# Performance work log

Hardware: AMD Instinct MI355X
Metric: run time of the kernel (lower is better)

The kernel has to match this reference:

```python
import jax, jax.numpy as jnp
import numpy as np

D_MODEL = 1024
N_HEADS = 16
HEAD_DIM = D_MODEL // N_HEADS


def setup_inputs() -> dict:
    key = jax.random.key(0)
    k1, k2, k3, k4, k5 = jax.random.split(key, 5)
    B, S = 2, 2048
    x = jax.random.normal(k1, (B, S, D_MODEL), dtype=jnp.float32)
    mask = jnp.ones((B, 1, S), dtype=jnp.int32)
    s1 = 1.0 / np.sqrt(D_MODEL)
    qkv_w = jax.random.normal(k2, (3 * D_MODEL, D_MODEL), dtype=jnp.float32) * s1
    qkv_b = jax.random.normal(k3, (3 * D_MODEL,), dtype=jnp.float32) * 0.02
    wo_w = jax.random.normal(k4, (D_MODEL, D_MODEL), dtype=jnp.float32) * s1
    wo_b = jax.random.normal(k5, (D_MODEL,), dtype=jnp.float32) * 0.02
    return {"x": x, "mask": mask, "qkv_w": qkv_w, "qkv_b": qkv_b, "wo_w": wo_w, "wo_b": wo_b}


def reference(x, mask, qkv_w, qkv_b, wo_w, wo_b):
    B, S, _ = x.shape
    # fused QKV projection: [B,S,3d]
    qkv = jnp.einsum('bsd,ed->bse', x, qkv_w) + qkv_b
    qkv = qkv.reshape(B, S, 3, N_HEADS, HEAD_DIM).transpose(2, 0, 3, 1, 4)
    q, k, v = qkv[0], qkv[1], qkv[2]  # each [B,H,S,hd]
    scores = jnp.einsum('bhsd,bhtd->bhst', q, k) / np.sqrt(HEAD_DIM)
    # mask [B,1,S] -> [B,1,1,S]; fill -inf where mask == 0
    scores = jnp.where(mask[:, None] == 0, -jnp.inf, scores)
    weights = jax.nn.softmax(scores, axis=-1)  # dropout p=0.0 -> identity
    out = jnp.einsum('bhst,bhtd->bhsd', weights, v)
    out = out.transpose(0, 2, 1, 3).reshape(B, S, D_MODEL)
    out = jnp.einsum('bsd,ed->bse', out, wo_w) + wo_b
    return out, weights
```

## Files before the change

### kernel.cpp

```cpp
#include <hip/hip_runtime.h>
#include <cstdint>
#include <cstddef>

typedef unsigned short u16;
typedef __attribute__((ext_vector_type(8))) short bf16x8;
typedef __attribute__((ext_vector_type(4))) float f32x4;

#define DEV static __device__ __forceinline__

DEV void gload_lds16(const void* g, void* l) {
  __builtin_amdgcn_global_load_lds((const __attribute__((address_space(1))) void*)g,
                                   (__attribute__((address_space(3))) void*)l, 16, 0, 0);
}

DEV u16 f2bf(float f) {
  unsigned x = __float_as_uint(f);
  return (u16)((x + 0x7FFFu + ((x >> 16) & 1u)) >> 16);
}

DEV unsigned cvtpk(float lo, float hi) {
  unsigned r;
  asm("v_cvt_pk_bf16_f32 %0, %1, %2" : "=v"(r) : "v"(lo), "v"(hi));
  return r;
}

#if __has_builtin(__builtin_amdgcn_exp2f)
DEV float fexp2(float x) { return __builtin_amdgcn_exp2f(x); }
#else
DEV float fexp2(float x) { return exp2f(x); }
#endif

#define WAITV(n)                                                   \
  do {                                                             \
    asm volatile("s_waitcnt vmcnt(" #n ")" ::: "memory");          \
    __builtin_amdgcn_sched_barrier(0);                             \
  } while (0)

DEV void sbar() {
  __builtin_amdgcn_sched_barrier(0);
  __builtin_amdgcn_s_barrier();
  __builtin_amdgcn_sched_barrier(0);
}

__global__ __launch_bounds__(256) void cvt3(const float* __restrict__ a, u16* __restrict__ da,
                                            const float* __restrict__ b, u16* __restrict__ db,
                                            const float* __restrict__ c, u16* __restrict__ dc,
                                            const int* __restrict__ mask,
                                            unsigned* __restrict__ mpack) {
  int bid = blockIdx.x;
  if (bid == 8192) {
    const int j = threadIdx.x;
    if (j < 128) {
      const int* mb = mask + (j >> 6) * 2048 + (j & 63) * 32;
      unsigned bits = 0;
      for (int k = 0; k < 32; ++k) bits |= (mb[k] != 0 ? 1u : 0u) << k;
      mpack[j] = bits;
    }
    return;
  }
  const float* s;
  u16* d;
  int base;
  if (bid < 4096) { s = a; d = da; base = bid; }
  else if (bid < 7168) { s = b; d = db; base = bid - 4096; }
  else { s = c; d = dc; base = bid - 7168; }
  const int i = (base * 256 + (int)threadIdx.x) * 4;
  float4 v = *(const float4*)(s + i);
  uint2 p;
  p.x = (unsigned)f2bf(v.x) | ((unsigned)f2bf(v.y) << 16);
  p.y = (unsigned)f2bf(v.z) | ((unsigned)f2bf(v.w) << 16);
  *(uint2*)(d + i) = p;
}

template <int EPI, int BM, int BN>
__global__ __launch_bounds__(256) void gemm_bt(const u16* __restrict__ A,
                                               const u16* __restrict__ Bm,
                                               const float* __restrict__ bias,
                                               void* __restrict__ Cout,
                                               u16* __restrict__ Vt,
                                               int M, int N, int K) {
  __shared__ u16 As[2][BM * 32];
  __shared__ u16 Bs[2][BN * 32];
  constexpr int MT = BM / 32, NT = BN / 32;
  const int cpx = (int)gridDim.x >> 3;
  const int bid = ((int)blockIdx.x & 7) * cpx + ((int)blockIdx.x >> 3);
  const int nb = N / BN;
  const int m0 = (bid / nb) * BM;
  const int n0 = (bid % nb) * BN;
  const int tid = threadIdx.x;
  const int w = tid >> 6, lane = tid & 63;
  const int wm = (w >> 1) * (BM / 2), wn = (w & 1) * (BN / 2);
  const int lr = lane & 15, lg = lane >> 4;

  f32x4 acc[MT][NT];
  const f32x4 z4 = {0.f, 0.f, 0.f, 0.f};
#pragma unroll
  for (int m = 0; m < MT; ++m)
#pragma unroll
    for (int n = 0; n < NT; ++n) acc[m][n] = z4;

  auto stage = [&](int ks, int buf) {
    const int k0 = ks << 5;
#pragma unroll
    for (int i = 0; i < BM * 4 / 256; ++i) {
      const int o = i * 256 + tid;
      const int row = o >> 2, c = o & 3;
      gload_lds16(A + (size_t)(m0 + row) * K + k0 + c * 8, &As[buf][(i * 256 + w * 64) * 8]);
    }
#pragma unroll
    for (int i = 0; i < BN * 4 / 256; ++i) {
      const int o = i * 256 + tid;
      const int row = o >> 2, c = o & 3;
      gload_lds16(Bm + (size_t)(n0 + row) * K + k0 + c * 8, &Bs[buf][(i * 256 + w * 64) * 8]);
    }
  };

  const int nk = K >> 5;
  stage(0, 0);
  __syncthreads();
  for (int ks = 0; ks < nk; ++ks) {
    const int cur = ks & 1;
    if (ks + 1 < nk) stage(ks + 1, cur ^ 1);
    bf16x8 af[MT], bfr[NT];
#pragma unroll
    for (int m = 0; m < MT; ++m)
      af[m] = *(const bf16x8*)&As[cur][(wm + m * 16 + lr) * 32 + lg * 8];
#pragma unroll
    for (int n = 0; n < NT; ++n)
      bfr[n] = *(const bf16x8*)&Bs[cur][(wn + n * 16 + lr) * 32 + lg * 8];
    __builtin_amdgcn_s_setprio(1);
#pragma unroll
    for (int m = 0; m < MT; ++m)
#pragma unroll
      for (int n = 0; n < NT; ++n)
        acc[m][n] = __builtin_amdgcn_mfma_f32_16x16x32_bf16(af[m], bfr[n], acc[m][n], 0, 0, 0);
    __builtin_amdgcn_s_setprio(0);
    __syncthreads();
  }

#pragma unroll
  for (int n = 0; n < NT; ++n) {
    const int e = n0 + wn + n * 16 + lr;
    const float bv = bias[e];
    if (EPI == 1 && (e >> 10) == 2) {
      const int h = (e >> 6) & 15, d = e & 63;
#pragma unroll
      for (int m = 0; m < MT; ++m) {
        const int row0 = m0 + wm + m * 16 + lg * 4;
        const int bb = row0 >> 11, s0 = row0 & 2047;
        uint2 pv;
        pv.x = cvtpk(acc[m][n][0] + bv, acc[m][n][1] + bv);
        pv.y = cvtpk(acc[m][n][2] + bv, acc[m][n][3] + bv);
        *(uint2*)(Vt + (size_t)(bb * 16 + h) * 131072 + (size_t)d * 2048 + s0) = pv;
      }
    } else {
#pragma unroll
      for (int m = 0; m < MT; ++m) {
#pragma unroll
        for (int r = 0; r < 4; ++r) {
          const int row = m0 + wm + m * 16 + lg * 4 + r;
          const float v = acc[m][n][r] + bv;
          if (EPI == 0) {
            ((float*)Cout)[(size_t)row * N + e] = v;
          } else {
            const int which = e >> 10, h = (e >> 6) & 15, d = e & 63;
            const int bb = row >> 11, s = row & 2047;
            ((u16*)Cout)[(size_t)which * 4194304 +
                         (((size_t)(bb * 16 + h) * 2048 + s) << 6) + d] = f2bf(v);
          }
        }
      }
    }
  }
}

__global__ __launch_bounds__(256, 4) void attn(const u16* __restrict__ Q,
                                               const u16* __restrict__ Kg,
                                               const u16* __restrict__ Vtg,
                                               const unsigned* __restrict__ mpack,
                                               float* __restrict__ Wout,
                                               u16* __restrict__ Og) {
  __shared__ u16 Ks[2][4096];
  __shared__ u16 Vs[2][4096];
  __shared__ float Pf[4][512];
  const int L = ((int)blockIdx.x & 7) * 128 + ((int)blockIdx.x >> 3);
  const int bh = L >> 5, qt = L & 31;
  const int b = bh >> 4, h = bh & 15;
  const int tid = threadIdx.x;
  const int w = tid >> 6, lane = tid & 63;
  const int lr = lane & 15, lg = lane >> 4;
  const int srow0 = qt * 64 + w * 16;
  const float C2 = 0.18033688011112042f;
  const float M2 = 11.541560327111707f;

  const u16* qrow = Q + ((size_t)bh * 2048 + srow0 + lr) * 64;
  const bf16x8 qf0 = *(const bf16x8*)(qrow + lg * 8);
  const bf16x8 qf1 = *(const bf16x8*)(qrow + 32 + lg * 8);
  const unsigned* mpk = mpack + b * 64;

  auto stageK = [&](int kt, u16* dst) {
    const u16* g = Kg + (size_t)bh * 131072 + (size_t)kt * 4096;
#pragma unroll
    for (int iss = 0; iss < 2; ++iss) {
      const int o = iss * 256 + tid;
      const int row = o >> 3, c = o & 7;
      gload_lds16(g + row * 64 + ((c ^ (row & 7)) << 3), dst + (iss * 256 + w * 64) * 8);
    }
  };
  auto stageV = [&](int kt, u16* dst) {
    const u16* g = Vtg + (size_t)bh * 131072 + kt * 64;
#pragma unroll
    for (int iss = 0; iss < 2; ++iss) {
      const int o = iss * 256 + tid;
      const int row = o >> 3, c = o & 7;
      gload_lds16(g + (size_t)row * 2048 + ((c ^ (row & 7)) << 3),
                  dst + (iss * 256 + w * 64) * 8);
    }
  };
  auto qk = [&](const u16* kb, f32x4* sc) {
    const f32x4 z4 = {0.f, 0.f, 0.f, 0.f};
    __builtin_amdgcn_s_setprio(1);
#pragma unroll
    for (int n = 0; n < 4; ++n) {
      const int tr = n * 16 + lr;
      const bf16x8 k0 = *(const bf16x8*)&kb[tr * 64 + ((lg ^ (tr & 7)) << 3)];
      const bf16x8 k1 = *(const bf16x8*)&kb[tr * 64 + (((lg + 4) ^ (tr & 7)) << 3)];
      f32x4 s = z4;
      s = __builtin_amdgcn_mfma_f32_16x16x32_bf16(k0, qf0, s, 0, 0, 0);
      s = __builtin_amdgcn_mfma_f32_16x16x32_bf16(k1, qf1, s, 0, 0, 0);
      sc[n] = s;
    }
    __builtin_amdgcn_s_setprio(0);
  };

  stageK(0, &Ks[0][0]);
  stageK(1, &Ks[1][0]);
  WAITV(2);
  sbar();
  float lsum = 0.f;
  int cur3 = 0, stg3 = 2;
  for (int t = 0; t < 32; ++t) {
    u16* curb = (cur3 == 0) ? &Ks[0][0] : ((cur3 == 1) ? &Ks[1][0] : &Vs[0][0]);
    const unsigned mx = mpk[t * 2], my = mpk[t * 2 + 1];
    if (t + 2 < 32) {
      u16* stb = (stg3 == 0) ? &Ks[0][0] : ((stg3 == 1) ? &Ks[1][0] : &Vs[0][0]);
      stageK(t + 2, stb);
    }
    f32x4 sc[4];
    qk(curb, sc);
    f32x4 p[4];
#pragma unroll
    for (int n = 0; n < 4; ++n)
#pragma unroll
      for (int r = 0; r < 4; ++r) p[n][r] = fexp2(fmaf(sc[n][r], C2, -M2));
    if ((mx & my) != 0xFFFFFFFFu) {
#pragma unroll
      for (int n = 0; n < 4; ++n) {
        const unsigned wsel = (n < 2) ? mx : my;
#pragma unroll
        for (int r = 0; r < 4; ++r) {
          const unsigned bit = (wsel >> ((n & 1) * 16 + lg * 4 + r)) & 1u;
          p[n][r] = bit ? p[n][r] : 0.f;
        }
      }
    }
#pragma unroll
    for (int n = 0; n < 4; ++n) lsum += (p[n][0] + p[n][1]) + (p[n][2] + p[n][3]);
    if (t + 1 < 32) {
      if (t + 2 < 32) {
        WAITV(2);
      } else {
        WAITV(0);
      }
      sbar();
    }
    cur3 = (cur3 == 2) ? 0 : cur3 + 1;
    stg3 = (stg3 == 2) ? 0 : stg3 + 1;
  }
  lsum += __shfl_xor(lsum, 16);
  lsum += __shfl_xor(lsum, 32);
  const float rl = 1.0f / lsum;

  sbar();
  f32x4 oacc[4];
  const f32x4 z4 = {0.f, 0.f, 0.f, 0.f};
#pragma unroll
  for (int n = 0; n < 4; ++n) oacc[n] = z4;

  float* Wb = Wout + (size_t)bh * 2048 * 2048;
  char* pfw = (char*)&Pf[w][0];
  const int sw = (lr & 7) << 4;
  const int ql0 = lane >> 3, ch = lane & 7;

  stageK(0, &Ks[0][0]);
  stageV(0, &Vs[0][0]);
  WAITV(0);
  sbar();
  for (int t = 0; t < 32; ++t) {
    const int cur = t & 1;
    const unsigned mx = mpk[t * 2], my = mpk[t * 2 + 1];
    if (t + 1 < 32) {
      stageK(t + 1, &Ks[cur ^ 1][0]);
      stageV(t + 1, &Vs[cur ^ 1][0]);
    }
    f32x4 sc[4];
    qk(&Ks[cur][0], sc);
    f32x4 wv[4];
#pragma unroll
    for (int n = 0; n < 4; ++n)
#pragma unroll
      for (int r = 0; r < 4; ++r) wv[n][r] = fexp2(fmaf(sc[n][r], C2, -M2)) * rl;
    if ((mx & my) != 0xFFFFFFFFu) {
#pragma unroll
      for (int n = 0; n < 4; ++n) {
        const unsigned wsel = (n < 2) ? mx : my;
#pragma unroll
        for (int r = 0; r < 4; ++r) {
          const unsigned bit = (wsel >> ((n & 1) * 16 + lg * 4 + r)) & 1u;
          wv[n][r] = bit ? wv[n][r] : 0.f;
        }
      }
    }
#pragma unroll
    for (int hh = 0; hh < 2; ++hh) {
      *(f32x4*)(pfw + (lr * 128 + ((lg * 16) ^ sw))) = wv[2 * hh];
      *(f32x4*)(pfw + (lr * 128 + ((64 + lg * 16) ^ sw))) = wv[2 * hh + 1];
#pragma unroll
      for (int s2 = 0; s2 < 2; ++s2) {
        const int ql = s2 * 8 + ql0;
        const f32x4 rv = *(const f32x4*)(pfw + (ql * 128 + ((ch * 16) ^ ((ql & 7) << 4))));
        __builtin_nontemporal_store(
            rv, (f32x4*)(Wb + (size_t)(srow0 + ql) * 2048 + t * 64 + hh * 32 + ch * 4));
      }
      const f32x4 a0 = *(const f32x4*)(pfw + (lr * 128 + ((lg * 32) ^ sw)));
      const f32x4 a1 = *(const f32x4*)(pfw + (lr * 128 + ((lg * 32 + 16) ^ sw)));
      int4 pk4;
      pk4.x = cvtpk(a0[0], a0[1]);
      pk4.y = cvtpk(a0[2], a0[3]);
      pk4.z = cvtpk(a1[0], a1[1]);
      pk4.w = cvtpk(a1[2], a1[3]);
      const bf16x8 pfr = *(const bf16x8*)&pk4;
      __builtin_amdgcn_s_setprio(1);
#pragma unroll
      for (int n = 0; n < 4; ++n) {
        const int dr = n * 16 + lr;
        const bf16x8 vf = *(const bf16x8*)&Vs[cur][dr * 64 + (((lg + hh * 4) ^ (dr & 7)) << 3)];
        oacc[n] = __builtin_amdgcn_mfma_f32_16x16x32_bf16(pfr, vf, oacc[n], 0, 0, 0);
      }
      __builtin_amdgcn_s_setprio(0);
    }
    if (t + 1 < 32) {
      WAITV(4);
      sbar();
    }
  }

#pragma unroll
  for (int n = 0; n < 4; ++n)
#pragma unroll
    for (int r = 0; r < 4; ++r) {
      const int s = srow0 + lg * 4 + r;
      Og[((size_t)(b * 2048 + s)) * 1024 + h * 64 + n * 16 + lr] = f2bf(oacc[n][r]);
    }
}

extern "C" void kernel_launch(void* const* d_in, const int* in_sizes, int n_in,
                              void* d_out, int out_size, void* d_ws, size_t ws_size,
                              hipStream_t stream) {
  const float* x     = (const float*)d_in[0];
  const int*   mask  = (const int*)d_in[1];
  const float* qkv_w = (const float*)d_in[2];
  const float* qkv_b = (const float*)d_in[3];
  const float* wo_w  = (const float*)d_in[4];
  const float* wo_b  = (const float*)d_in[5];
  float* out = (float*)d_out;

  char* ws = (char*)d_ws;
  u16* xb   = (u16*)(ws);
  u16* qwb  = (u16*)(ws + (8u << 20));
  u16* wob  = (u16*)(ws + (14u << 20));
  u16* qkvb = (u16*)(ws + (16u << 20));
  unsigned* mpack = (unsigned*)(ws + (16u << 20) + 16777216);
  u16* vt   = (u16*)(ws + (40u << 20));
  u16* ob   = (u16*)(ws + (48u << 20));

  cvt3<<<8193, 256, 0, stream>>>(x, xb, qkv_w, qwb, wo_w, wob, mask, mpack);
  gemm_bt<1, 128, 128><<<768, 256, 0, stream>>>(xb, qwb, qkv_b, qkvb, vt, 4096, 3072, 1024);
  attn<<<1024, 256, 0, stream>>>(qkvb, qkvb + 4194304, vt, mpack, out + 4194304, ob);
  gemm_bt<0, 128, 64><<<512, 256, 0, stream>>>(ob, wob, wo_b, out, nullptr, 4096, 1024, 1024);
}
```

Baseline: 201.6 us.

## Process two query tiles per attention block, fusing tile B's row-sum into tile A's pass

Each attention block now handles two 64-row query tiles instead of one, halving the grid. The first tile's softmax denominator pass stages K in 128-row chunks. Its output pass also computes the second tile's row sums from the same K loads, which removes one full K sweep per pair of tiles. The trade-offs are a smaller grid and lower occupancy (launch bounds cut from 4 to 2), more register pressure, and three serialized K sweeps per block.

```diff
diff --git a/kernel.cpp b/kernel.cpp
--- a/kernel.cpp
+++ b/kernel.cpp
@@ -174,30 +174,43 @@
   }
 }
 
-__global__ __launch_bounds__(256, 4) void attn(const u16* __restrict__ Q,
+__global__ __launch_bounds__(256, 2) void attn(const u16* __restrict__ Q,
                                                const u16* __restrict__ Kg,
                                                const u16* __restrict__ Vtg,
                                                const unsigned* __restrict__ mpack,
                                                float* __restrict__ Wout,
                                                u16* __restrict__ Og) {
-  __shared__ u16 Ks[2][4096];
-  __shared__ u16 Vs[2][4096];
+  __shared__ u16 SM[16384];
   __shared__ float Pf[4][512];
-  const int L = ((int)blockIdx.x & 7) * 128 + ((int)blockIdx.x >> 3);
-  const int bh = L >> 5, qt = L & 31;
+  const int L = ((int)blockIdx.x & 7) * 64 + ((int)blockIdx.x >> 3);
+  const int bh = L >> 4, pair = L & 15;
   const int b = bh >> 4, h = bh & 15;
   const int tid = threadIdx.x;
   const int w = tid >> 6, lane = tid & 63;
   const int lr = lane & 15, lg = lane >> 4;
-  const int srow0 = qt * 64 + w * 16;
+  const int sr_a = pair * 128 + w * 16;
+  const int sr_b = sr_a + 64;
   const float C2 = 0.18033688011112042f;
   const float M2 = 11.541560327111707f;
-
-  const u16* qrow = Q + ((size_t)bh * 2048 + srow0 + lr) * 64;
-  const bf16x8 qf0 = *(const bf16x8*)(qrow + lg * 8);
-  const bf16x8 qf1 = *(const bf16x8*)(qrow + 32 + lg * 8);
+  const f32x4 z4 = {0.f, 0.f, 0.f, 0.f};
+
+  const u16* qra = Q + ((size_t)bh * 2048 + sr_a + lr) * 64;
+  const u16* qrb = qra + 64 * 64;
+  const bf16x8 qfa0 = *(const bf16x8*)(qra + lg * 8);
+  const bf16x8 qfa1 = *(const bf16x8*)(qra + 32 + lg * 8);
+  const bf16x8 qfb0 = *(const bf16x8*)(qrb + lg * 8);
+  const bf16x8 qfb1 = *(const bf16x8*)(qrb + 32 + lg * 8);
   const unsigned* mpk = mpack + b * 64;
 
+  auto stageC = [&](int ch, u16* dst) {
+    const u16* g = Kg + (size_t)bh * 131072 + (size_t)ch * 8192;
+#pragma unroll
+    for (int iss = 0; iss < 4; ++iss) {
+      const int o = iss * 256 + tid;
+      const int row = o >> 3, c = o & 7;
+      gload_lds16(g + row * 64 + ((c ^ (row & 7)) << 3), dst + (iss * 256 + w * 64) * 8);
+    }
+  };
   auto stageK = [&](int kt, u16* dst) {
     const u16* g = Kg + (size_t)bh * 131072 + (size_t)kt * 4096;
 #pragma unroll
@@ -217,8 +230,7 @@
                   dst + (iss * 256 + w * 64) * 8);
     }
   };
-  auto qk = [&](const u16* kb, f32x4* sc) {
-    const f32x4 z4 = {0.f, 0.f, 0.f, 0.f};
+  auto qk1 = [&](const u16* kb, const bf16x8& q0, const bf16x8& q1, f32x4* sc) {
     __builtin_amdgcn_s_setprio(1);
 #pragma unroll
     for (int n = 0; n < 4; ++n) {
@@ -226,33 +238,13 @@
       const bf16x8 k0 = *(const bf16x8*)&kb[tr * 64 + ((lg ^ (tr & 7)) << 3)];
       const bf16x8 k1 = *(const bf16x8*)&kb[tr * 64 + (((lg + 4) ^ (tr & 7)) << 3)];
       f32x4 s = z4;
-      s = __builtin_amdgcn_mfma_f32_16x16x32_bf16(k0, qf0, s, 0, 0, 0);
-      s = __builtin_amdgcn_mfma_f32_16x16x32_bf16(k1, qf1, s, 0, 0, 0);
+      s = __builtin_amdgcn_mfma_f32_16x16x32_bf16(k0, q0, s, 0, 0, 0);
+      s = __builtin_amdgcn_mfma_f32_16x16x32_bf16(k1, q1, s, 0, 0, 0);
       sc[n] = s;
     }
     __builtin_amdgcn_s_setprio(0);
   };
-
-  stageK(0, &Ks[0][0]);
-  stageK(1, &Ks[1][0]);
-  WAITV(2);
-  sbar();
-  float lsum = 0.f;
-  int cur3 = 0, stg3 = 2;
-  for (int t = 0; t < 32; ++t) {
-    u16* curb = (cur3 == 0) ? &Ks[0][0] : ((cur3 == 1) ? &Ks[1][0] : &Vs[0][0]);
-    const unsigned mx = mpk[t * 2], my = mpk[t * 2 + 1];
-    if (t + 2 < 32) {
-      u16* stb = (stg3 == 0) ? &Ks[0][0] : ((stg3 == 1) ? &Ks[1][0] : &Vs[0][0]);
-      stageK(t + 2, stb);
-    }
-    f32x4 sc[4];
-    qk(curb, sc);
-    f32x4 p[4];
-#pragma unroll
-    for (int n = 0; n < 4; ++n)
-#pragma unroll
-      for (int r = 0; r < 4; ++r) p[n][r] = fexp2(fmaf(sc[n][r], C2, -M2));
+  auto maskp = [&](unsigned mx, unsigned my, f32x4* p) {
     if ((mx & my) != 0xFFFFFFFFu) {
 #pragma unroll
       for (int n = 0; n < 4; ++n) {
@@ -264,63 +256,13 @@
         }
       }
     }
-#pragma unroll
-    for (int n = 0; n < 4; ++n) lsum += (p[n][0] + p[n][1]) + (p[n][2] + p[n][3]);
-    if (t + 1 < 32) {
-      if (t + 2 < 32) {
-        WAITV(2);
-      } else {
-        WAITV(0);
-      }
-      sbar();
-    }
-    cur3 = (cur3 == 2) ? 0 : cur3 + 1;
-    stg3 = (stg3 == 2) ? 0 : stg3 + 1;
-  }
-  lsum += __shfl_xor(lsum, 16);
-  lsum += __shfl_xor(lsum, 32);
-  const float rl = 1.0f / lsum;
-
-  sbar();
-  f32x4 oacc[4];
-  const f32x4 z4 = {0.f, 0.f, 0.f, 0.f};
-#pragma unroll
-  for (int n = 0; n < 4; ++n) oacc[n] = z4;
-
-  float* Wb = Wout + (size_t)bh * 2048 * 2048;
+  };
+
   char* pfw = (char*)&Pf[w][0];
   const int sw = (lr & 7) << 4;
-  const int ql0 = lane >> 3, ch = lane & 7;
-
-  stageK(0, &Ks[0][0]);
-  stageV(0, &Vs[0][0]);
-  WAITV(0);
-  sbar();
-  for (int t = 0; t < 32; ++t) {
-    const int cur = t & 1;
-    const unsigned mx = mpk[t * 2], my = mpk[t * 2 + 1];
-    if (t + 1 < 32) {
-      stageK(t + 1, &Ks[cur ^ 1][0]);
-      stageV(t + 1, &Vs[cur ^ 1][0]);
-    }
-    f32x4 sc[4];
-    qk(&Ks[cur][0], sc);
-    f32x4 wv[4];
-#pragma unroll
-    for (int n = 0; n < 4; ++n)
-#pragma unroll
-      for (int r = 0; r < 4; ++r) wv[n][r] = fexp2(fmaf(sc[n][r], C2, -M2)) * rl;
-    if ((mx & my) != 0xFFFFFFFFu) {
-#pragma unroll
-      for (int n = 0; n < 4; ++n) {
-        const unsigned wsel = (n < 2) ? mx : my;
-#pragma unroll
-        for (int r = 0; r < 4; ++r) {
-          const unsigned bit = (wsel >> ((n & 1) * 16 + lg * 4 + r)) & 1u;
-          wv[n][r] = bit ? wv[n][r] : 0.f;
-        }
-      }
-    }
+  const int ql0 = lane >> 3, ch8 = lane & 7;
+
+  auto p2tail = [&](int t, const u16* vb, f32x4* wv, float* Wb0, f32x4* oacc) {
 #pragma unroll
     for (int hh = 0; hh < 2; ++hh) {
       *(f32x4*)(pfw + (lr * 128 + ((lg * 16) ^ sw))) = wv[2 * hh];
@@ -328,9 +270,9 @@
 #pragma unroll
       for (int s2 = 0; s2 < 2; ++s2) {
         const int ql = s2 * 8 + ql0;
-        const f32x4 rv = *(const f32x4*)(pfw + (ql * 128 + ((ch * 16) ^ ((ql & 7) << 4))));
+        const f32x4 rv = *(const f32x4*)(pfw + (ql * 128 + ((ch8 * 16) ^ ((ql & 7) << 4))));
         __builtin_nontemporal_store(
-            rv, (f32x4*)(Wb + (size_t)(srow0 + ql) * 2048 + t * 64 + hh * 32 + ch * 4));
+            rv, (f32x4*)(Wb0 + (size_t)ql * 2048 + t * 64 + hh * 32 + ch8 * 4));
       }
       const f32x4 a0 = *(const f32x4*)(pfw + (lr * 128 + ((lg * 32) ^ sw)));
       const f32x4 a1 = *(const f32x4*)(pfw + (lr * 128 + ((lg * 32 + 16) ^ sw)));
@@ -344,22 +286,148 @@
 #pragma unroll
       for (int n = 0; n < 4; ++n) {
         const int dr = n * 16 + lr;
-        const bf16x8 vf = *(const bf16x8*)&Vs[cur][dr * 64 + (((lg + hh * 4) ^ (dr & 7)) << 3)];
+        const bf16x8 vf = *(const bf16x8*)&vb[dr * 64 + (((lg + hh * 4) ^ (dr & 7)) << 3)];
         oacc[n] = __builtin_amdgcn_mfma_f32_16x16x32_bf16(pfr, vf, oacc[n], 0, 0, 0);
       }
       __builtin_amdgcn_s_setprio(0);
     }
+  };
+
+  float lsa = 0.f;
+  stageC(0, &SM[0]);
+  WAITV(0);
+  sbar();
+  for (int r = 0; r < 16; ++r) {
+    const u16* cb = &SM[(r & 1) * 8192];
+    const unsigned m0_ = mpk[r * 4], m1_ = mpk[r * 4 + 1];
+    const unsigned m2_ = mpk[r * 4 + 2], m3_ = mpk[r * 4 + 3];
+    if (r + 1 < 16) stageC(r + 1, &SM[((r + 1) & 1) * 8192]);
+#pragma unroll
+    for (int hh = 0; hh < 2; ++hh) {
+      f32x4 sc[4];
+      qk1(cb + hh * 4096, qfa0, qfa1, sc);
+      f32x4 p[4];
+#pragma unroll
+      for (int n = 0; n < 4; ++n)
+#pragma unroll
+        for (int rr = 0; rr < 4; ++rr) p[n][rr] = fexp2(fmaf(sc[n][rr], C2, -M2));
+      maskp(hh ? m2_ : m0_, hh ? m3_ : m1_, p);
+#pragma unroll
+      for (int n = 0; n < 4; ++n) lsa += (p[n][0] + p[n][1]) + (p[n][2] + p[n][3]);
+    }
+    if (r + 1 < 16) {
+      WAITV(0);
+      sbar();
+    }
+  }
+  lsa += __shfl_xor(lsa, 16);
+  lsa += __shfl_xor(lsa, 32);
+  const float rl_a = 1.0f / lsa;
+  sbar();
+
+  f32x4 oacc[4];
+#pragma unroll
+  for (int n = 0; n < 4; ++n) oacc[n] = z4;
+  float lsb = 0.f;
+  float* Wba = Wout + ((size_t)bh * 2048 + sr_a) * 2048;
+  float* Wbb = Wout + ((size_t)bh * 2048 + sr_b) * 2048;
+
+  stageK(0, &SM[0]);
+  stageV(0, &SM[8192]);
+  WAITV(0);
+  sbar();
+  for (int t = 0; t < 32; ++t) {
+    const int cur = t & 1;
+    const u16* kb = &SM[cur * 4096];
+    const u16* vb = &SM[8192 + cur * 4096];
+    const unsigned mx = mpk[t * 2], my = mpk[t * 2 + 1];
+    if (t + 1 < 32) {
+      stageK(t + 1, &SM[(cur ^ 1) * 4096]);
+      stageV(t + 1, &SM[8192 + (cur ^ 1) * 4096]);
+    }
+    f32x4 sa[4], sb[4];
+    __builtin_amdgcn_s_setprio(1);
+#pragma unroll
+    for (int n = 0; n < 4; ++n) {
+      const int tr = n * 16 + lr;
+      const bf16x8 k0 = *(const bf16x8*)&kb[tr * 64 + ((lg ^ (tr & 7)) << 3)];
+      const bf16x8 k1 = *(const bf16x8*)&kb[tr * 64 + (((lg + 4) ^ (tr & 7)) << 3)];
+      f32x4 s = z4;
+      s = __builtin_amdgcn_mfma_f32_16x16x32_bf16(k0, qfa0, s, 0, 0, 0);
+      s = __builtin_amdgcn_mfma_f32_16x16x32_bf16(k1, qfa1, s, 0, 0, 0);
+      sa[n] = s;
+      f32x4 s2 = z4;
+      s2 = __builtin_amdgcn_mfma_f32_16x16x32_bf16(k0, qfb0, s2, 0, 0, 0);
+      s2 = __builtin_amdgcn_mfma_f32_16x16x32_bf16(k1, qfb1, s2, 0, 0, 0);
+      sb[n] = s2;
+    }
+    __builtin_amdgcn_s_setprio(0);
+    f32x4 wv[4], pb[4];
+#pragma unroll
+    for (int n = 0; n < 4; ++n)
+#pragma unroll
+      for (int rr = 0; rr < 4; ++rr) {
+        wv[n][rr] = fexp2(fmaf(sa[n][rr], C2, -M2)) * rl_a;
+        pb[n][rr] = fexp2(fmaf(sb[n][rr], C2, -M2));
+      }
+    if ((mx & my) != 0xFFFFFFFFu) {
+      maskp(mx, my, wv);
+      maskp(mx, my, pb);
+    }
+#pragma unroll
+    for (int n = 0; n < 4; ++n) lsb += (pb[n][0] + pb[n][1]) + (pb[n][2] + pb[n][3]);
+    p2tail(t, vb, wv, Wba, oacc);
     if (t + 1 < 32) {
       WAITV(4);
       sbar();
     }
   }
-
+  lsb += __shfl_xor(lsb, 16);
+  lsb += __shfl_xor(lsb, 32);
+  const float rl_b = 1.0f / lsb;
 #pragma unroll
   for (int n = 0; n < 4; ++n)
 #pragma unroll
     for (int r = 0; r < 4; ++r) {
-      const int s = srow0 + lg * 4 + r;
+      const int s = sr_a + lg * 4 + r;
+      Og[((size_t)(b * 2048 + s)) * 1024 + h * 64 + n * 16 + lr] = f2bf(oacc[n][r]);
+    }
+  sbar();
+
+#pragma unroll
+  for (int n = 0; n < 4; ++n) oacc[n] = z4;
+  stageK(0, &SM[0]);
+  stageV(0, &SM[8192]);
+  WAITV(0);
+  sbar();
+  for (int t = 0; t < 32; ++t) {
+    const int cur = t & 1;
+    const u16* kb = &SM[cur * 4096];
+    const u16* vb = &SM[8192 + cur * 4096];
+    const unsigned mx = mpk[t * 2], my = mpk[t * 2 + 1];
+    if (t + 1 < 32) {
+      stageK(t + 1, &SM[(cur ^ 1) * 4096]);
+      stageV(t + 1, &SM[8192 + (cur ^ 1) * 4096]);
+    }
+    f32x4 sc[4];
+    qk1(kb, qfb0, qfb1, sc);
+    f32x4 wv[4];
+#pragma unroll
+    for (int n = 0; n < 4; ++n)
+#pragma unroll
+      for (int rr = 0; rr < 4; ++rr) wv[n][rr] = fexp2(fmaf(sc[n][rr], C2, -M2)) * rl_b;
+    maskp(mx, my, wv);
+    p2tail(t, vb, wv, Wbb, oacc);
+    if (t + 1 < 32) {
+      WAITV(4);
+      sbar();
+    }
+  }
+#pragma unroll
+  for (int n = 0; n < 4; ++n)
+#pragma unroll
+    for (int r = 0; r < 4; ++r) {
+      const int s = sr_b + lg * 4 + r;
       Og[((size_t)(b * 2048 + s)) * 1024 + h * 64 + n * 16 + lr] = f2bf(oacc[n][r]);
     }
 }
@@ -386,6 +454,6 @@
 
   cvt3<<<8193, 256, 0, stream>>>(x, xb, qkv_w, qwb, wo_w, wob, mask, mpack);
   gemm_bt<1, 128, 128><<<768, 256, 0, stream>>>(xb, qwb, qkv_b, qkvb, vt, 4096, 3072, 1024);
-  attn<<<1024, 256, 0, stream>>>(qkvb, qkvb + 4194304, vt, mpack, out + 4194304, ob);
+  attn<<<512, 256, 0, stream>>>(qkvb, qkvb + 4194304, vt, mpack, out + 4194304, ob);
   gemm_bt<0, 128, 64><<<512, 256, 0, stream>>>(ob, wob, wo_b, out, nullptr, 4096, 1024, 1024);
 }
```

Result: no change. 199.1 us (-1.2%).
